# Kernel optimization log

Measured on AMD Instinct MI355X. Metric: run time of the kernel, lower is better.

## Reference

```python
import jax, jax.numpy as jnp
import numpy as np

B, H, L, D, BLK = 2, 16, 2048, 64, 32
NB = L // BLK          # 64 blocks per side
WINDOW = 8             # causal local window, in blocks


def make_layout():
    # [H, NB, NB] int32: block (i, j) active iff 0 <= i - j < WINDOW (causal local band)
    bi = jnp.arange(NB)
    band = ((bi[:, None] - bi[None, :]) >= 0) & ((bi[:, None] - bi[None, :]) < WINDOW)
    return jnp.broadcast_to(band[None].astype(jnp.int32), (H, NB, NB))


def setup_inputs() -> dict:
    rng = jax.random.key(0)
    kq, kk, kv, kp = jax.random.split(rng, 4)
    return {
        "query": jax.random.normal(kq, (B, H, L, D), dtype=jnp.float32),
        "key": jax.random.normal(kk, (B, H, L, D), dtype=jnp.float32),
        "value": jax.random.normal(kv, (B, H, L, D), dtype=jnp.float32),
        "key_padding_mask": jax.random.normal(kp, (B, L), dtype=jnp.float32),
        "layout": make_layout(),
    }


def reference(query, key, value, key_padding_mask, layout):
    # query/key/value: [B, H, L, D]; layout: [H, NB, NB] block sparsity pattern
    bsz, num_heads, tgt_len, head_dim = query.shape
    blk = tgt_len // layout.shape[1]
    scaling = float(head_dim) ** (-0.5)

    # SDD: scores only on active blocks. Reference computes dense then masks
    # inactive blocks to -inf, matching blocksparse softmax semantics exactly.
    scores = jnp.einsum("bhqd,bhkd->bhqk", query, key) * scaling
    # key_padding_mask_mode='add': added to logits, broadcast over queries
    scores = scores + key_padding_mask[:, None, None, :]

    # expand block layout [H, NB, NB] -> element mask [H, L, L]
    block_mask = jnp.repeat(jnp.repeat(layout.astype(bool), blk, axis=1), blk, axis=2)
    scores = jnp.where(block_mask[None], scores, -jnp.inf)

    probs = jax.nn.softmax(scores, axis=-1)  # zeros outside active blocks
    # DSD: probs @ value
    attn_output = jnp.einsum("bhqk,bhkd->bhqd", probs, value)
    return attn_output
```

## Files before the change

### kernel.cpp

```cpp
#include <hip/hip_runtime.h>

#define B_   2
#define H_   16
#define L_   2048
#define D_   64
#define BLK_ 32
#define NB_  64

#define KSW 64
#define VS  40
#define PS  40

typedef __bf16 bf16x8 __attribute__((ext_vector_type(8)));
typedef float  f32x4  __attribute__((ext_vector_type(4)));
typedef unsigned short u16x8 __attribute__((ext_vector_type(8)));

__device__ inline unsigned short f2bf(float f) {
    unsigned int u = __builtin_bit_cast(unsigned int, f);
    unsigned int r = u + 0x7fffu + ((u >> 16) & 1u);
    return (unsigned short)(r >> 16);
}

#define WG_BARRIER() asm volatile("s_waitcnt lgkmcnt(0)\n\ts_barrier" ::: "memory")

struct Tile {
    float4 k0, k1;
    float  v[8];
    float  kp0, kp1;
};

__global__ __launch_bounds__(256, 4)
void sparse_attn_kernel(const float* __restrict__ qg,
                        const float* __restrict__ kg,
                        const float* __restrict__ vg,
                        const float* __restrict__ kpm,
                        const int*   __restrict__ layout,
                        float* __restrict__ outg)
{
    __shared__ __align__(16) unsigned short Ks_[2][BLK_ * KSW];
    __shared__ __align__(16) unsigned short Vt_[2][D_ * VS];
    __shared__ __align__(16) unsigned short Ps_[4][16 * PS];

    const int tid  = threadIdx.x;
    const int wave = tid >> 6;
    const int lane = tid & 63;
    const int quad = lane >> 4;
    const int l15  = lane & 15;

    const int phys = blockIdx.x;
    const int lw   = (phys & 7) * 128 + (phys >> 3);
    const int ip = lw & 31;
    const int h  = (lw >> 5) & 15;
    const int b  = lw >> 9;
    const int i0 = ip * 2, i1 = i0 + 1;
    const int iq = i0 + (wave >> 1);

    const size_t bh = (size_t)(b * H_ + h);
    const float* kbase  = kg  + bh * L_ * D_;
    const float* vbase  = vg  + bh * L_ * D_;
    const float* kpb    = kpm + (size_t)b * L_;
    const int*   layrow = layout + (h * NB_ + iq) * NB_;

    const int jbeg = i0 - 7;

    int act[9];
    #pragma unroll
    for (int s = 0; s < 9; ++s) {
        const int j = jbeg + s;
        act[s] = (j >= 0) ? layrow[j] : 0;
    }

    bf16x8 aq[2];
    {
        const int gq = iq * BLK_ + (wave & 1) * 16 + l15;
        const float* qrow = qg + (bh * L_ + gq) * D_;
        #pragma unroll
        for (int ks = 0; ks < 2; ++ks) {
            float4 x = *(const float4*)&qrow[ks * 32 + quad * 8];
            float4 y = *(const float4*)&qrow[ks * 32 + quad * 8 + 4];
            u16x8 pk;
            pk[0]=f2bf(x.x); pk[1]=f2bf(x.y); pk[2]=f2bf(x.z); pk[3]=f2bf(x.w);
            pk[4]=f2bf(y.x); pk[5]=f2bf(y.y); pk[6]=f2bf(y.z); pk[7]=f2bf(y.w);
            aq[ks] = __builtin_bit_cast(bf16x8, pk);
        }
    }

    auto clampj = [&](int j) { return j < 0 ? 0 : j; };

    auto loadT = [&](int jc, Tile& T) {
        const float4* kb = (const float4*)(kbase + (size_t)jc * BLK_ * D_);
        T.k0 = kb[tid * 2];
        T.k1 = kb[tid * 2 + 1];
        const float* vb = vbase + (size_t)jc * BLK_ * D_;
        #pragma unroll
        for (int i = 0; i < 8; ++i) T.v[i] = vb[(wave * 8 + i) * D_ + lane];
        T.kp0 = kpb[jc * BLK_ + l15];
        T.kp1 = kpb[jc * BLK_ + 16 + l15];
    };

    auto storeT = [&](int buf, const Tile& T) {
        const int row = tid >> 3, oct = tid & 7;
        u16x8 pk;
        pk[0]=f2bf(T.k0.x); pk[1]=f2bf(T.k0.y); pk[2]=f2bf(T.k0.z); pk[3]=f2bf(T.k0.w);
        pk[4]=f2bf(T.k1.x); pk[5]=f2bf(T.k1.y); pk[6]=f2bf(T.k1.z); pk[7]=f2bf(T.k1.w);
        *(u16x8*)&Ks_[buf][row * KSW + ((oct ^ (row & 7)) * 8)] = pk;
        u16x8 pv;
        #pragma unroll
        for (int i = 0; i < 8; ++i) pv[i] = f2bf(T.v[i]);
        *(u16x8*)&Vt_[buf][lane * VS + ((wave ^ (lane & 3)) * 8)] = pv;
    };

    float lrow[4] = {0.f, 0.f, 0.f, 0.f};
    f32x4 Ot[4];
    #pragma unroll
    for (int t = 0; t < 4; ++t) Ot[t] = (f32x4){0.f, 0.f, 0.f, 0.f};

    auto computeT = [&](int buf, float kp0c, float kp1c) {
        f32x4 s0 = {0.f,0.f,0.f,0.f}, s1 = {0.f,0.f,0.f,0.f};
        #pragma unroll
        for (int ks = 0; ks < 2; ++ks) {
            const int so = ((ks * 4 + quad) ^ (l15 & 7)) * 8;
            bf16x8 b0 = *(const bf16x8*)&Ks_[buf][l15 * KSW + so];
            bf16x8 b1 = *(const bf16x8*)&Ks_[buf][(16 + l15) * KSW + so];
            s0 = __builtin_amdgcn_mfma_f32_16x16x32_bf16(aq[ks], b0, s0, 0, 0, 0);
            s1 = __builtin_amdgcn_mfma_f32_16x16x32_bf16(aq[ks], b1, s1, 0, 0, 0);
        }
        unsigned short* psw = &Ps_[wave][0];
        #pragma unroll
        for (int r = 0; r < 4; ++r) {
            float p0 = __expf(s0[r] * 0.125f + kp0c);
            float p1 = __expf(s1[r] * 0.125f + kp1c);
            lrow[r] += p0 + p1;
            const int prow = quad * 4 + r;
            psw[prow * PS + l15]      = f2bf(p0);
            psw[prow * PS + 16 + l15] = f2bf(p1);
        }
        asm volatile("s_waitcnt lgkmcnt(0)" ::: "memory");
        bf16x8 ap = *(const bf16x8*)&psw[l15 * PS + quad * 8];
        #pragma unroll
        for (int t = 0; t < 4; ++t) {
            bf16x8 bv = *(const bf16x8*)&Vt_[buf][(t * 16 + l15) * VS + ((quad ^ (l15 & 3)) * 8)];
            Ot[t] = __builtin_amdgcn_mfma_f32_16x16x32_bf16(ap, bv, Ot[t], 0, 0, 0);
        }
    };

    Tile tiles[2];
    loadT(clampj(jbeg), tiles[0]);
    storeT(0, tiles[0]);
    float kp0c = tiles[0].kp0, kp1c = tiles[0].kp1;
    loadT(clampj(jbeg + 1), tiles[1]);
    WG_BARRIER();

    int cur = 0;
    #pragma unroll
    for (int s = 0; s < 9; ++s) {
        const int j = jbeg + s;
        if (s <= 6) loadT(clampj(j + 2), tiles[s & 1]);
        if (act[s] != 0) computeT(cur, kp0c, kp1c);
        if (s < 8) {
            const Tile& T = tiles[(s + 1) & 1];
            storeT(cur ^ 1, T);
            kp0c = T.kp0; kp1c = T.kp1;
        }
        WG_BARRIER();
        cur ^= 1;
    }

    #pragma unroll
    for (int r = 0; r < 4; ++r) {
        #pragma unroll
        for (int m = 1; m < 16; m <<= 1) lrow[r] += __shfl_xor(lrow[r], m);
    }
    float* ob = outg + (bh * L_ + (size_t)iq * BLK_ + (wave & 1) * 16) * D_;
    #pragma unroll
    for (int r = 0; r < 4; ++r) {
        float inv = 1.0f / lrow[r];
        int prow = quad * 4 + r;
        #pragma unroll
        for (int t = 0; t < 4; ++t)
            ob[prow * D_ + t * 16 + l15] = Ot[t][r] * inv;
    }
}

extern "C" void kernel_launch(void* const* d_in, const int* in_sizes, int n_in,
                              void* d_out, int out_size, void* d_ws, size_t ws_size,
                              hipStream_t stream) {
    const float* q      = (const float*)d_in[0];
    const float* k      = (const float*)d_in[1];
    const float* v      = (const float*)d_in[2];
    const float* kpmask = (const float*)d_in[3];
    const int*   layout = (const int*)d_in[4];
    float* out = (float*)d_out;

    dim3 grid(B_ * H_ * (NB_ / 2));
    dim3 block(256);
    sparse_attn_kernel<<<grid, block, 0, stream>>>(q, k, v, kpmask, layout, out);
}
```

Before: 102.8 us.

## Use one query block per workgroup and keep probabilities in registers via transposed MFMA

Each workgroup now handles a single query block with 2 waves, replacing the old pair of query blocks with 4 waves, and the grid doubles to match. The score MFMA is transposed so the bf16 probabilities land directly in the B-operand layout for the PV MFMA, which removes the per-wave P staging through LDS. K and V are converted to bf16 at load time, and the output is staged through LDS so it can be written with float4 stores. The cost is that K/V tiles are no longer shared across two query blocks, and the iteration count drops from 9 to 8 per block.

```diff
diff --git a/kernel.cpp b/kernel.cpp
--- a/kernel.cpp
+++ b/kernel.cpp
@@ -9,10 +9,11 @@
 
 #define KSW 64
 #define VS  40
-#define PS  40
+#define OS  65
 
 typedef __bf16 bf16x8 __attribute__((ext_vector_type(8)));
 typedef float  f32x4  __attribute__((ext_vector_type(4)));
+typedef unsigned short u16x4 __attribute__((ext_vector_type(4)));
 typedef unsigned short u16x8 __attribute__((ext_vector_type(8)));
 
 __device__ inline unsigned short f2bf(float f) {
@@ -20,16 +21,15 @@
     unsigned int r = u + 0x7fffu + ((u >> 16) & 1u);
     return (unsigned short)(r >> 16);
 }
-
 #define WG_BARRIER() asm volatile("s_waitcnt lgkmcnt(0)\n\ts_barrier" ::: "memory")
 
 struct Tile {
-    float4 k0, k1;
-    float  v[8];
-    float  kp0, kp1;
+    u16x8  kc0, kc1;
+    u16x4  vg[4];
+    float4 kpa, kpb;
 };
 
-__global__ __launch_bounds__(256, 4)
+__global__ __launch_bounds__(128, 4)
 void sparse_attn_kernel(const float* __restrict__ qg,
                         const float* __restrict__ kg,
                         const float* __restrict__ vg,
@@ -37,9 +37,13 @@
                         const int*   __restrict__ layout,
                         float* __restrict__ outg)
 {
-    __shared__ __align__(16) unsigned short Ks_[2][BLK_ * KSW];
-    __shared__ __align__(16) unsigned short Vt_[2][D_ * VS];
-    __shared__ __align__(16) unsigned short Ps_[4][16 * PS];
+    __shared__ __align__(16) union {
+        struct {
+            unsigned short Ks[2][BLK_ * KSW];
+            unsigned short Vt[2][D_ * VS];
+        } s;
+        float Os[32 * OS];
+    } Lds;
 
     const int tid  = threadIdx.x;
     const int wave = tid >> 6;
@@ -48,32 +52,28 @@
     const int l15  = lane & 15;
 
     const int phys = blockIdx.x;
-    const int lw   = (phys & 7) * 128 + (phys >> 3);
-    const int ip = lw & 31;
-    const int h  = (lw >> 5) & 15;
-    const int b  = lw >> 9;
-    const int i0 = ip * 2, i1 = i0 + 1;
-    const int iq = i0 + (wave >> 1);
+    const int lw   = (phys & 7) * 256 + (phys >> 3);
+    const int i = lw & 63;
+    const int h = (lw >> 6) & 15;
+    const int b = lw >> 10;
 
     const size_t bh = (size_t)(b * H_ + h);
-    const float* kbase  = kg  + bh * L_ * D_;
-    const float* vbase  = vg  + bh * L_ * D_;
-    const float* kpb    = kpm + (size_t)b * L_;
-    const int*   layrow = layout + (h * NB_ + iq) * NB_;
-
-    const int jbeg = i0 - 7;
-
-    int act[9];
-    #pragma unroll
-    for (int s = 0; s < 9; ++s) {
+    const float* kbase = kg + bh * L_ * D_;
+    const float* vbase = vg + bh * L_ * D_;
+    const float* kpp   = kpm + (size_t)b * L_;
+    const int*   layrow = layout + (h * NB_ + i) * NB_;
+
+    const int jbeg = i - 7;
+    int act[8];
+    #pragma unroll
+    for (int s = 0; s < 8; ++s) {
         const int j = jbeg + s;
         act[s] = (j >= 0) ? layrow[j] : 0;
     }
 
     bf16x8 aq[2];
     {
-        const int gq = iq * BLK_ + (wave & 1) * 16 + l15;
-        const float* qrow = qg + (bh * L_ + gq) * D_;
+        const float* qrow = qg + (bh * L_ + (size_t)i * BLK_ + wave * 16 + l15) * D_;
         #pragma unroll
         for (int ks = 0; ks < 2; ++ks) {
             float4 x = *(const float4*)&qrow[ks * 32 + quad * 8];
@@ -88,97 +88,116 @@
     auto clampj = [&](int j) { return j < 0 ? 0 : j; };
 
     auto loadT = [&](int jc, Tile& T) {
-        const float4* kb = (const float4*)(kbase + (size_t)jc * BLK_ * D_);
-        T.k0 = kb[tid * 2];
-        T.k1 = kb[tid * 2 + 1];
+        const float* kb = kbase + (size_t)jc * BLK_ * D_;
+        float4 a0 = *(const float4*)&kb[tid * 8];
+        float4 a1 = *(const float4*)&kb[tid * 8 + 4];
+        float4 b0 = *(const float4*)&kb[(tid + 128) * 8];
+        float4 b1 = *(const float4*)&kb[(tid + 128) * 8 + 4];
+        u16x8 k0, k1;
+        k0[0]=f2bf(a0.x); k0[1]=f2bf(a0.y); k0[2]=f2bf(a0.z); k0[3]=f2bf(a0.w);
+        k0[4]=f2bf(a1.x); k0[5]=f2bf(a1.y); k0[6]=f2bf(a1.z); k0[7]=f2bf(a1.w);
+        k1[0]=f2bf(b0.x); k1[1]=f2bf(b0.y); k1[2]=f2bf(b0.z); k1[3]=f2bf(b0.w);
+        k1[4]=f2bf(b1.x); k1[5]=f2bf(b1.y); k1[6]=f2bf(b1.z); k1[7]=f2bf(b1.w);
+        T.kc0 = k0; T.kc1 = k1;
         const float* vb = vbase + (size_t)jc * BLK_ * D_;
         #pragma unroll
-        for (int i = 0; i < 8; ++i) T.v[i] = vb[(wave * 8 + i) * D_ + lane];
-        T.kp0 = kpb[jc * BLK_ + l15];
-        T.kp1 = kpb[jc * BLK_ + 16 + l15];
+        for (int g = 0; g < 4; ++g) {
+            u16x4 pv;
+            #pragma unroll
+            for (int r = 0; r < 4; ++r)
+                pv[r] = f2bf(vb[(wave * 16 + g * 4 + r) * D_ + lane]);
+            T.vg[g] = pv;
+        }
+        T.kpa = *(const float4*)&kpp[jc * BLK_ + quad * 4];
+        T.kpb = *(const float4*)&kpp[jc * BLK_ + 16 + quad * 4];
     };
 
     auto storeT = [&](int buf, const Tile& T) {
         const int row = tid >> 3, oct = tid & 7;
-        u16x8 pk;
-        pk[0]=f2bf(T.k0.x); pk[1]=f2bf(T.k0.y); pk[2]=f2bf(T.k0.z); pk[3]=f2bf(T.k0.w);
-        pk[4]=f2bf(T.k1.x); pk[5]=f2bf(T.k1.y); pk[6]=f2bf(T.k1.z); pk[7]=f2bf(T.k1.w);
-        *(u16x8*)&Ks_[buf][row * KSW + ((oct ^ (row & 7)) * 8)] = pk;
-        u16x8 pv;
-        #pragma unroll
-        for (int i = 0; i < 8; ++i) pv[i] = f2bf(T.v[i]);
-        *(u16x8*)&Vt_[buf][lane * VS + ((wave ^ (lane & 3)) * 8)] = pv;
+        *(u16x8*)&Lds.s.Ks[buf][row * KSW + ((oct ^ (row & 7)) * 8)]        = T.kc0;
+        *(u16x8*)&Lds.s.Ks[buf][(16 + row) * KSW + ((oct ^ (row & 7)) * 8)] = T.kc1;
+        const int swz = lane & 3;
+        const int wo  = wave * 4;
+        #pragma unroll
+        for (int g = 0; g < 4; ++g)
+            *(u16x4*)&Lds.s.Vt[buf][lane * VS + ((g ^ swz) * 8) + wo] = T.vg[g];
     };
 
-    float lrow[4] = {0.f, 0.f, 0.f, 0.f};
+    float lsum = 0.f;
     f32x4 Ot[4];
     #pragma unroll
     for (int t = 0; t < 4; ++t) Ot[t] = (f32x4){0.f, 0.f, 0.f, 0.f};
 
-    auto computeT = [&](int buf, float kp0c, float kp1c) {
-        f32x4 s0 = {0.f,0.f,0.f,0.f}, s1 = {0.f,0.f,0.f,0.f};
+    auto computeT = [&](int buf, const float4& kp0, const float4& kp1) {
+        f32x4 st0 = {0.f,0.f,0.f,0.f}, st1 = {0.f,0.f,0.f,0.f};
         #pragma unroll
         for (int ks = 0; ks < 2; ++ks) {
-            const int so = ((ks * 4 + quad) ^ (l15 & 7)) * 8;
-            bf16x8 b0 = *(const bf16x8*)&Ks_[buf][l15 * KSW + so];
-            bf16x8 b1 = *(const bf16x8*)&Ks_[buf][(16 + l15) * KSW + so];
-            s0 = __builtin_amdgcn_mfma_f32_16x16x32_bf16(aq[ks], b0, s0, 0, 0, 0);
-            s1 = __builtin_amdgcn_mfma_f32_16x16x32_bf16(aq[ks], b1, s1, 0, 0, 0);
-        }
-        unsigned short* psw = &Ps_[wave][0];
+            const int co = (((ks * 4 + quad) ^ (l15 & 7)) * 8);
+            bf16x8 ka  = *(const bf16x8*)&Lds.s.Ks[buf][l15 * KSW + co];
+            bf16x8 kb2 = *(const bf16x8*)&Lds.s.Ks[buf][(16 + l15) * KSW + co];
+            st0 = __builtin_amdgcn_mfma_f32_16x16x32_bf16(ka,  aq[ks], st0, 0, 0, 0);
+            st1 = __builtin_amdgcn_mfma_f32_16x16x32_bf16(kb2, aq[ks], st1, 0, 0, 0);
+        }
+        u16x8 bpk;
         #pragma unroll
         for (int r = 0; r < 4; ++r) {
-            float p0 = __expf(s0[r] * 0.125f + kp0c);
-            float p1 = __expf(s1[r] * 0.125f + kp1c);
-            lrow[r] += p0 + p1;
-            const int prow = quad * 4 + r;
-            psw[prow * PS + l15]      = f2bf(p0);
-            psw[prow * PS + 16 + l15] = f2bf(p1);
-        }
-        asm volatile("s_waitcnt lgkmcnt(0)" ::: "memory");
-        bf16x8 ap = *(const bf16x8*)&psw[l15 * PS + quad * 8];
+            float p0 = __expf(st0[r] * 0.125f + kp0[r]);
+            float p1 = __expf(st1[r] * 0.125f + kp1[r]);
+            lsum += p0 + p1;
+            bpk[r]     = f2bf(p0);
+            bpk[4 + r] = f2bf(p1);
+        }
+        bf16x8 bp = __builtin_bit_cast(bf16x8, bpk);
+        const int swzv = l15 & 3;
         #pragma unroll
         for (int t = 0; t < 4; ++t) {
-            bf16x8 bv = *(const bf16x8*)&Vt_[buf][(t * 16 + l15) * VS + ((quad ^ (l15 & 3)) * 8)];
-            Ot[t] = __builtin_amdgcn_mfma_f32_16x16x32_bf16(ap, bv, Ot[t], 0, 0, 0);
+            bf16x8 av = *(const bf16x8*)&Lds.s.Vt[buf][(t * 16 + l15) * VS + ((quad ^ swzv) * 8)];
+            Ot[t] = __builtin_amdgcn_mfma_f32_16x16x32_bf16(av, bp, Ot[t], 0, 0, 0);
         }
     };
 
     Tile tiles[2];
     loadT(clampj(jbeg), tiles[0]);
     storeT(0, tiles[0]);
-    float kp0c = tiles[0].kp0, kp1c = tiles[0].kp1;
+    float4 kpc0 = tiles[0].kpa, kpc1 = tiles[0].kpb;
     loadT(clampj(jbeg + 1), tiles[1]);
     WG_BARRIER();
 
     int cur = 0;
     #pragma unroll
-    for (int s = 0; s < 9; ++s) {
+    for (int s = 0; s < 8; ++s) {
         const int j = jbeg + s;
-        if (s <= 6) loadT(clampj(j + 2), tiles[s & 1]);
-        if (act[s] != 0) computeT(cur, kp0c, kp1c);
-        if (s < 8) {
+        if (s <= 5) loadT(clampj(j + 2), tiles[s & 1]);
+        if (act[s] != 0) computeT(cur, kpc0, kpc1);
+        if (s < 7) {
             const Tile& T = tiles[(s + 1) & 1];
             storeT(cur ^ 1, T);
-            kp0c = T.kp0; kp1c = T.kp1;
+            kpc0 = T.kpa; kpc1 = T.kpb;
         }
         WG_BARRIER();
         cur ^= 1;
     }
 
-    #pragma unroll
-    for (int r = 0; r < 4; ++r) {
-        #pragma unroll
-        for (int m = 1; m < 16; m <<= 1) lrow[r] += __shfl_xor(lrow[r], m);
-    }
-    float* ob = outg + (bh * L_ + (size_t)iq * BLK_ + (wave & 1) * 16) * D_;
-    #pragma unroll
-    for (int r = 0; r < 4; ++r) {
-        float inv = 1.0f / lrow[r];
-        int prow = quad * 4 + r;
-        #pragma unroll
-        for (int t = 0; t < 4; ++t)
-            ob[prow * D_ + t * 16 + l15] = Ot[t][r] * inv;
+    lsum += __shfl_xor(lsum, 16);
+    lsum += __shfl_xor(lsum, 32);
+    const float rinv = 1.0f / lsum;
+
+    float* osw = &Lds.Os[(wave * 16) * OS];
+    #pragma unroll
+    for (int t = 0; t < 4; ++t)
+        #pragma unroll
+        for (int r = 0; r < 4; ++r)
+            osw[l15 * OS + t * 16 + quad * 4 + r] = Ot[t][r] * rinv;
+    asm volatile("s_waitcnt lgkmcnt(0)" ::: "memory");
+
+    const int qrow = lane >> 2, sc = lane & 3;
+    float* outp = outg + (bh * L_ + (size_t)i * BLK_ + wave * 16) * D_;
+    #pragma unroll
+    for (int c = 0; c < 4; ++c) {
+        float4 gv;
+        #pragma unroll
+        for (int r = 0; r < 4; ++r) gv[r] = osw[qrow * OS + c * 16 + sc * 4 + r];
+        *(float4*)&outp[qrow * D_ + c * 16 + sc * 4] = gv;
     }
 }
 
@@ -192,7 +211,7 @@
     const int*   layout = (const int*)d_in[4];
     float* out = (float*)d_out;
 
-    dim3 grid(B_ * H_ * (NB_ / 2));
-    dim3 block(256);
+    dim3 grid(B_ * H_ * NB_);
+    dim3 block(128);
     sparse_attn_kernel<<<grid, block, 0, stream>>>(q, k, v, kpmask, layout, out);
 }
```

After: 129.3 us. 1.26x slower.
